# Optimization experiments

Hardware: AMD Instinct MI355X
Metric: run time of the kernel (lower is better)

## Reference

```python
import jax, jax.numpy as jnp
import numpy as np

P, N, C_IN, UNITS = 40000, 32, 4, 64
VX, VY = 0.2, 0.2
X_OFF = VX / 2 + 0.0      # pc_range x_min = 0
Y_OFF = VY / 2 + (-40.0)  # pc_range y_min = -40
BN_EPS = 1e-3


def setup_inputs() -> dict:
    key = jax.random.key(0)
    k1, k2, k3, k4, k5 = jax.random.split(key, 5)
    features = jax.random.normal(k1, (P, N, C_IN), dtype=jnp.float32)
    num_voxels = jax.random.randint(k2, (P,), 1, N + 1, dtype=jnp.int32)
    yx = jax.random.randint(k3, (P, 2), 0, 350, dtype=jnp.int32)
    coors = jnp.concatenate([jnp.zeros((P, 2), jnp.int32), yx], axis=1)  # (batch, z, y, x)
    W = jax.random.normal(k4, (C_IN + 5, UNITS), dtype=jnp.float32) * 0.1
    gamma = jnp.ones((UNITS,), jnp.float32)
    beta = jnp.zeros((UNITS,), jnp.float32)
    return {"features": features, "num_voxels": num_voxels, "coors": coors,
            "W": W, "gamma": gamma, "beta": beta}


def _pfn_forward(features, num_voxels, coors, W, gamma, beta):
    dtype = features.dtype
    nv = num_voxels.astype(dtype)[:, None, None]                      # [P,1,1]
    points_mean = jnp.sum(features[:, :, :3], axis=1, keepdims=True) / nv
    f_cluster = features[:, :, :3] - points_mean                      # [P,N,3]
    fx = features[:, :, 0] - (coors[:, 3].astype(dtype)[:, None] * VX + X_OFF)
    fy = features[:, :, 1] - (coors[:, 2].astype(dtype)[:, None] * VY + Y_OFF)
    f_center = jnp.stack([fx, fy], axis=-1)                           # [P,N,2]
    feats = jnp.concatenate([features, f_cluster, f_center], axis=-1) # [P,N,9]
    # mask out padded points (n >= num_voxels)
    mask = (jnp.arange(N)[None, :] < num_voxels[:, None]).astype(dtype)[..., None]
    feats = feats * mask
    # PFNLayer: linear (no bias) -> BN1d (training-mode batch stats) -> relu -> max over points
    x = jnp.einsum('pnc,cu->pnu', feats, W)                           # [P,N,U]
    mean = jnp.mean(x, axis=(0, 1))
    var = jnp.mean(jnp.square(x - mean), axis=(0, 1))                 # biased, as torch BN
    x = (x - mean) * jax.lax.rsqrt(var + BN_EPS) * gamma + beta
    x = jax.nn.relu(x)
    return jnp.max(x, axis=1)                                         # [P,U] (squeezed)


def reference(features, num_voxels, coors, W, gamma, beta):
    return _pfn_forward(features, num_voxels, coors, W, gamma, beta)
```

## Files before the change

kernel.cpp:

```cpp
#include <hip/hip_runtime.h>
#include <math.h>

#define NPTS   32
#define UNITS  64
#define PTOT   40000
#define NPAIRS (PTOT / 2)
#define SBLOCKS 2500
#define WPB     4
#define TOTW    (SBLOCKS * WPB)
#define PPW     (NPAIRS / TOTW)


__global__ __launch_bounds__(256)
void pfn_main(const float* __restrict__ feat,
              const int*   __restrict__ nvox,
              const int*   __restrict__ coors,
              const float* __restrict__ Wm,
              const float* __restrict__ gamma,
              float*       __restrict__ xext,
              float*       __restrict__ partials)
{
    __shared__ float ps[WPB][128];

    const int tid  = threadIdx.x;
    const int lane = tid & 63;
    const int wave = __builtin_amdgcn_readfirstlane(tid >> 6);
    const int gwave = blockIdx.x * WPB + wave;

    const float sg  = (gamma[lane] >= 0.f) ? 1.f : -1.f;
    const float w4 = sg * Wm[4 * UNITS + lane], w5 = sg * Wm[5 * UNITS + lane];
    const float w6 = sg * Wm[6 * UNITS + lane], w7 = sg * Wm[7 * UNITS + lane];
    const float w8 = sg * Wm[8 * UNITS + lane];
    const float wp0 = sg * Wm[0 * UNITS + lane] + w4 + w7;
    const float wp1 = sg * Wm[1 * UNITS + lane] + w5 + w8;
    const float wp2 = sg * Wm[2 * UNITS + lane] + w6;
    const float wp3 = sg * Wm[3 * UNITS + lane];

    float lsum = 0.f, lsq = 0.f;

    #pragma unroll
    for (int it = 0; it < PPW; ++it) {
        const int pair = it * TOTW + gwave;
        const int p0 = pair * 2;

        const float4 f4 = *reinterpret_cast<const float4*>(feat + (size_t)pair * 256 + lane * 4);
        float sx = f4.x, sy = f4.y, sz = f4.z;
        #pragma unroll
        for (int off = 1; off < 32; off <<= 1) {
            sx += __shfl_xor(sx, off);
            sy += __shfl_xor(sy, off);
            sz += __shfl_xor(sz, off);
        }

        int nvA = nvox[p0], nvB = nvox[p0 + 1];
        nvA = nvA < 1 ? 1 : (nvA > NPTS ? NPTS : nvA);
        nvB = nvB < 1 ? 1 : (nvB > NPTS ? NPTS : nvB);
        const float cxA = (float)coors[p0 * 4 + 3] * 0.2f + 0.1f;
        const float cyA = (float)coors[p0 * 4 + 2] * 0.2f + (-39.9f);
        const float cxB = (float)coors[p0 * 4 + 7] * 0.2f + 0.1f;
        const float cyB = (float)coors[p0 * 4 + 6] * 0.2f + (-39.9f);
        const float iA  = 1.f / (float)nvA,  iB  = 1.f / (float)nvB;
        const float mA0 = __shfl(sx, 0)  * iA, mA1 = __shfl(sy, 0)  * iA, mA2 = __shfl(sz, 0)  * iA;
        const float mB0 = __shfl(sx, 32) * iB, mB1 = __shfl(sy, 32) * iB, mB2 = __shfl(sz, 32) * iB;
        const float bA = -(mA0 * w4 + mA1 * w5 + mA2 * w6 + cxA * w7 + cyA * w8);
        const float bB = -(mB0 * w4 + mB1 * w5 + mB2 * w6 + cxB * w7 + cyB * w8);

        const float* fpA = feat + (size_t)p0 * 128;
        const float* fpB = fpA + 128;

        float mA = -3.4e38f, mB = -3.4e38f;
        const int nmin = nvA < nvB ? nvA : nvB;

        #pragma unroll 4
        for (int n = 0; n < nmin; ++n) {
            const float4 a  = *reinterpret_cast<const float4*>(fpA + n * 4);
            const float4 b4 = *reinterpret_cast<const float4*>(fpB + n * 4);
            const float xA = fmaf(a.x,  wp0, fmaf(a.y,  wp1, fmaf(a.z,  wp2, fmaf(a.w,  wp3, bA))));
            const float xB = fmaf(b4.x, wp0, fmaf(b4.y, wp1, fmaf(b4.z, wp2, fmaf(b4.w, wp3, bB))));
            lsum += xA; lsq = fmaf(xA, xA, lsq); mA = fmaxf(mA, xA);
            lsum += xB; lsq = fmaf(xB, xB, lsq); mB = fmaxf(mB, xB);
        }
        #pragma unroll 4
        for (int n = nmin; n < nvA; ++n) {
            const float4 a = *reinterpret_cast<const float4*>(fpA + n * 4);
            const float xA = fmaf(a.x, wp0, fmaf(a.y, wp1, fmaf(a.z, wp2, fmaf(a.w, wp3, bA))));
            lsum += xA; lsq = fmaf(xA, xA, lsq); mA = fmaxf(mA, xA);
        }
        #pragma unroll 4
        for (int n = nmin; n < nvB; ++n) {
            const float4 b4 = *reinterpret_cast<const float4*>(fpB + n * 4);
            const float xB = fmaf(b4.x, wp0, fmaf(b4.y, wp1, fmaf(b4.z, wp2, fmaf(b4.w, wp3, bB))));
            lsum += xB; lsq = fmaf(xB, xB, lsq); mB = fmaxf(mB, xB);
        }

        xext[(size_t)p0 * UNITS + lane]       = sg * mA;
        xext[(size_t)(p0 + 1) * UNITS + lane] = sg * mB;
    }

    ps[wave][lane]      = sg * lsum;
    ps[wave][64 + lane] = lsq;
    __syncthreads();
    if (tid < 128)
        partials[blockIdx.x * 128 + tid] = ps[0][tid] + ps[1][tid] + ps[2][tid] + ps[3][tid];
}

__global__ __launch_bounds__(256)
void pfn_finalize(const float* __restrict__ partials,
                  const float* __restrict__ gamma,
                  const float* __restrict__ beta,
                  float*       __restrict__ ss)
{
    const int u = blockIdx.x;
    const int t = threadIdx.x;
    double aS = 0.0, aQ = 0.0;
    for (int b = t; b < SBLOCKS; b += 256) {
        aS += (double)partials[b * 128 + u];
        aQ += (double)partials[b * 128 + 64 + u];
    }
    __shared__ double sS[256], sQ[256];
    sS[t] = aS; sQ[t] = aQ;
    __syncthreads();
    for (int s = 128; s > 0; s >>= 1) {
        if (t < s) { sS[t] += sS[t + s]; sQ[t] += sQ[t + s]; }
        __syncthreads();
    }
    if (t == 0) {
        const double inv_pn = 1.0 / ((double)PTOT * (double)NPTS);
        const double mean = sS[0] * inv_pn;
        const double var  = sQ[0] * inv_pn - mean * mean;
        const float scale = gamma[u] * (float)(1.0 / sqrt(var + 1e-3));
        const float shift = beta[u] - (float)mean * scale;
        ss[u]      = scale;
        ss[64 + u] = shift;
    }
}

#define CBLOCKS 2500

__global__ __launch_bounds__(256)
void pfn_apply(const float4* __restrict__ xext,
               const int*    __restrict__ nvox,
               const float*  __restrict__ ss,
               float4*       __restrict__ out)
{
    const int i  = blockIdx.x * 256 + threadIdx.x;
    const int u0 = (i & 15) * 4;
    const int p  = i >> 4;
    const float4 sc = *reinterpret_cast<const float4*>(ss + u0);
    const float4 sh = *reinterpret_cast<const float4*>(ss + 64 + u0);
    const float4 e  = xext[i];
    const bool pad  = nvox[p] < NPTS;
    float4 o;
    o.x = fmaxf(fmaf(e.x, sc.x, sh.x), pad ? fmaxf(sh.x, 0.f) : 0.f);
    o.y = fmaxf(fmaf(e.y, sc.y, sh.y), pad ? fmaxf(sh.y, 0.f) : 0.f);
    o.z = fmaxf(fmaf(e.z, sc.z, sh.z), pad ? fmaxf(sh.z, 0.f) : 0.f);
    o.w = fmaxf(fmaf(e.w, sc.w, sh.w), pad ? fmaxf(sh.w, 0.f) : 0.f);
    out[i] = o;
}

extern "C" void kernel_launch(void* const* d_in, const int* in_sizes, int n_in,
                              void* d_out, int out_size, void* d_ws, size_t ws_size,
                              hipStream_t stream)
{
    const float* feat  = (const float*)d_in[0];
    const int*   nvox  = (const int*)d_in[1];
    const int*   coors = (const int*)d_in[2];
    const float* Wm    = (const float*)d_in[3];
    const float* gamma = (const float*)d_in[4];
    const float* beta  = (const float*)d_in[5];
    float* out = (float*)d_out;

    float* xext     = (float*)d_ws;
    float* partials = xext + (size_t)PTOT * UNITS;
    float* ss       = partials + (size_t)SBLOCKS * 128;

    pfn_main<<<SBLOCKS, 256, 0, stream>>>(feat, nvox, coors, Wm, gamma, xext, partials);
    pfn_finalize<<<UNITS, 256, 0, stream>>>(partials, gamma, beta, ss);
    pfn_apply<<<CBLOCKS, 256, 0, stream>>>((const float4*)xext, nvox, ss, (float4*)out);
}
```

Baseline: 34.73 us.

## Use readlane from registers, atomic stat accumulation, fold finalize into apply

The per-point inner loops now pull each point's features out of the already-loaded float4 register with readlane, instead of reloading them from global memory. The separate finalize kernel is removed. Block partial sums go into a 128-float accumulator through float atomics, cleared by a memset before the main kernel, and each apply block computes scale and shift in shared memory. This drops a kernel launch and redundant loads, but adds a memset node and 2500×128 contended atomics. It also switches the statistics to float32 accumulation with E[x²]−mean², which loses precision compared with the earlier double reduction.

```diff
diff --git a/kernel.cpp b/kernel.cpp
--- a/kernel.cpp
+++ b/kernel.cpp
@@ -1,15 +1,19 @@
 #include <hip/hip_runtime.h>
 #include <math.h>
 
-#define NPTS   32
-#define UNITS  64
-#define PTOT   40000
-#define NPAIRS (PTOT / 2)
+#define NPTS    32
+#define UNITS   64
+#define PTOT    40000
+#define NPAIRS  (PTOT / 2)
 #define SBLOCKS 2500
 #define WPB     4
 #define TOTW    (SBLOCKS * WPB)
 #define PPW     (NPAIRS / TOTW)
 
+
+__device__ __forceinline__ float rl(float v, int srclane) {
+    return __int_as_float(__builtin_amdgcn_readlane(__float_as_int(v), srclane));
+}
 
 __global__ __launch_bounds__(256)
 void pfn_main(const float* __restrict__ feat,
@@ -18,7 +22,7 @@
               const float* __restrict__ Wm,
               const float* __restrict__ gamma,
               float*       __restrict__ xext,
-              float*       __restrict__ partials)
+              float*       __restrict__ accum)
 {
     __shared__ float ps[WPB][128];
 
@@ -44,6 +48,7 @@
         const int p0 = pair * 2;
 
         const float4 f4 = *reinterpret_cast<const float4*>(feat + (size_t)pair * 256 + lane * 4);
+
         float sx = f4.x, sy = f4.y, sz = f4.z;
         #pragma unroll
         for (int off = 1; off < 32; off <<= 1) {
@@ -60,36 +65,37 @@
         const float cxB = (float)coors[p0 * 4 + 7] * 0.2f + 0.1f;
         const float cyB = (float)coors[p0 * 4 + 6] * 0.2f + (-39.9f);
         const float iA  = 1.f / (float)nvA,  iB  = 1.f / (float)nvB;
-        const float mA0 = __shfl(sx, 0)  * iA, mA1 = __shfl(sy, 0)  * iA, mA2 = __shfl(sz, 0)  * iA;
-        const float mB0 = __shfl(sx, 32) * iB, mB1 = __shfl(sy, 32) * iB, mB2 = __shfl(sz, 32) * iB;
+        const float mA0 = rl(sx, 0)  * iA, mA1 = rl(sy, 0)  * iA, mA2 = rl(sz, 0)  * iA;
+        const float mB0 = rl(sx, 32) * iB, mB1 = rl(sy, 32) * iB, mB2 = rl(sz, 32) * iB;
         const float bA = -(mA0 * w4 + mA1 * w5 + mA2 * w6 + cxA * w7 + cyA * w8);
         const float bB = -(mB0 * w4 + mB1 * w5 + mB2 * w6 + cxB * w7 + cyB * w8);
-
-        const float* fpA = feat + (size_t)p0 * 128;
-        const float* fpB = fpA + 128;
 
         float mA = -3.4e38f, mB = -3.4e38f;
         const int nmin = nvA < nvB ? nvA : nvB;
 
         #pragma unroll 4
         for (int n = 0; n < nmin; ++n) {
-            const float4 a  = *reinterpret_cast<const float4*>(fpA + n * 4);
-            const float4 b4 = *reinterpret_cast<const float4*>(fpB + n * 4);
-            const float xA = fmaf(a.x,  wp0, fmaf(a.y,  wp1, fmaf(a.z,  wp2, fmaf(a.w,  wp3, bA))));
-            const float xB = fmaf(b4.x, wp0, fmaf(b4.y, wp1, fmaf(b4.z, wp2, fmaf(b4.w, wp3, bB))));
+            const float aX = rl(f4.x, n),      aY = rl(f4.y, n);
+            const float aZ = rl(f4.z, n),      aW = rl(f4.w, n);
+            const float bX = rl(f4.x, n + 32), bY = rl(f4.y, n + 32);
+            const float bZ = rl(f4.z, n + 32), bW = rl(f4.w, n + 32);
+            const float xA = fmaf(aX, wp0, fmaf(aY, wp1, fmaf(aZ, wp2, fmaf(aW, wp3, bA))));
+            const float xB = fmaf(bX, wp0, fmaf(bY, wp1, fmaf(bZ, wp2, fmaf(bW, wp3, bB))));
             lsum += xA; lsq = fmaf(xA, xA, lsq); mA = fmaxf(mA, xA);
             lsum += xB; lsq = fmaf(xB, xB, lsq); mB = fmaxf(mB, xB);
         }
         #pragma unroll 4
         for (int n = nmin; n < nvA; ++n) {
-            const float4 a = *reinterpret_cast<const float4*>(fpA + n * 4);
-            const float xA = fmaf(a.x, wp0, fmaf(a.y, wp1, fmaf(a.z, wp2, fmaf(a.w, wp3, bA))));
+            const float aX = rl(f4.x, n), aY = rl(f4.y, n);
+            const float aZ = rl(f4.z, n), aW = rl(f4.w, n);
+            const float xA = fmaf(aX, wp0, fmaf(aY, wp1, fmaf(aZ, wp2, fmaf(aW, wp3, bA))));
             lsum += xA; lsq = fmaf(xA, xA, lsq); mA = fmaxf(mA, xA);
         }
         #pragma unroll 4
         for (int n = nmin; n < nvB; ++n) {
-            const float4 b4 = *reinterpret_cast<const float4*>(fpB + n * 4);
-            const float xB = fmaf(b4.x, wp0, fmaf(b4.y, wp1, fmaf(b4.z, wp2, fmaf(b4.w, wp3, bB))));
+            const float bX = rl(f4.x, n + 32), bY = rl(f4.y, n + 32);
+            const float bZ = rl(f4.z, n + 32), bW = rl(f4.w, n + 32);
+            const float xB = fmaf(bX, wp0, fmaf(bY, wp1, fmaf(bZ, wp2, fmaf(bW, wp3, bB))));
             lsum += xB; lsq = fmaf(xB, xB, lsq); mB = fmaxf(mB, xB);
         }
 
@@ -100,54 +106,40 @@
     ps[wave][lane]      = sg * lsum;
     ps[wave][64 + lane] = lsq;
     __syncthreads();
-    if (tid < 128)
-        partials[blockIdx.x * 128 + tid] = ps[0][tid] + ps[1][tid] + ps[2][tid] + ps[3][tid];
-}
-
-__global__ __launch_bounds__(256)
-void pfn_finalize(const float* __restrict__ partials,
-                  const float* __restrict__ gamma,
-                  const float* __restrict__ beta,
-                  float*       __restrict__ ss)
-{
-    const int u = blockIdx.x;
-    const int t = threadIdx.x;
-    double aS = 0.0, aQ = 0.0;
-    for (int b = t; b < SBLOCKS; b += 256) {
-        aS += (double)partials[b * 128 + u];
-        aQ += (double)partials[b * 128 + 64 + u];
-    }
-    __shared__ double sS[256], sQ[256];
-    sS[t] = aS; sQ[t] = aQ;
-    __syncthreads();
-    for (int s = 128; s > 0; s >>= 1) {
-        if (t < s) { sS[t] += sS[t + s]; sQ[t] += sQ[t + s]; }
-        __syncthreads();
-    }
-    if (t == 0) {
-        const double inv_pn = 1.0 / ((double)PTOT * (double)NPTS);
-        const double mean = sS[0] * inv_pn;
-        const double var  = sQ[0] * inv_pn - mean * mean;
-        const float scale = gamma[u] * (float)(1.0 / sqrt(var + 1e-3));
-        const float shift = beta[u] - (float)mean * scale;
-        ss[u]      = scale;
-        ss[64 + u] = shift;
+    if (tid < 128) {
+        const float v = ps[0][tid] + ps[1][tid] + ps[2][tid] + ps[3][tid];
+        atomicAdd(&accum[tid], v);
     }
 }
 
 #define CBLOCKS 2500
 
 __global__ __launch_bounds__(256)
-void pfn_apply(const float4* __restrict__ xext,
+void pfn_apply(const float*  __restrict__ accum,
+               const float*  __restrict__ gamma,
+               const float*  __restrict__ beta,
+               const float4* __restrict__ xext,
                const int*    __restrict__ nvox,
-               const float*  __restrict__ ss,
                float4*       __restrict__ out)
 {
-    const int i  = blockIdx.x * 256 + threadIdx.x;
+    __shared__ __align__(16) float s_sc[64], s_sh[64];
+    const int t = threadIdx.x;
+    if (t < 64) {
+        const float INV_PN = 1.0f / (float)(PTOT * NPTS);
+        const float S = accum[t], Q = accum[64 + t];
+        const float mean  = S * INV_PN;
+        const float var   = Q * INV_PN - mean * mean;
+        const float scale = gamma[t] * rsqrtf(var + 1e-3f);
+        s_sc[t] = scale;
+        s_sh[t] = beta[t] - mean * scale;
+    }
+    __syncthreads();
+
+    const int i  = blockIdx.x * 256 + t;
     const int u0 = (i & 15) * 4;
     const int p  = i >> 4;
-    const float4 sc = *reinterpret_cast<const float4*>(ss + u0);
-    const float4 sh = *reinterpret_cast<const float4*>(ss + 64 + u0);
+    const float4 sc = *reinterpret_cast<const float4*>(&s_sc[u0]);
+    const float4 sh = *reinterpret_cast<const float4*>(&s_sh[u0]);
     const float4 e  = xext[i];
     const bool pad  = nvox[p] < NPTS;
     float4 o;
@@ -170,11 +162,11 @@
     const float* beta  = (const float*)d_in[5];
     float* out = (float*)d_out;
 
-    float* xext     = (float*)d_ws;
-    float* partials = xext + (size_t)PTOT * UNITS;
-    float* ss       = partials + (size_t)SBLOCKS * 128;
+    float* xext  = (float*)d_ws;
+    float* accum = xext + (size_t)PTOT * UNITS;
 
-    pfn_main<<<SBLOCKS, 256, 0, stream>>>(feat, nvox, coors, Wm, gamma, xext, partials);
-    pfn_finalize<<<UNITS, 256, 0, stream>>>(partials, gamma, beta, ss);
-    pfn_apply<<<CBLOCKS, 256, 0, stream>>>((const float4*)xext, nvox, ss, (float4*)out);
+    hipMemsetAsync(accum, 0, 128 * sizeof(float), stream);
+    pfn_main<<<SBLOCKS, 256, 0, stream>>>(feat, nvox, coors, Wm, gamma, xext, accum);
+    pfn_apply<<<CBLOCKS, 256, 0, stream>>>(accum, gamma, beta,
+                                           (const float4*)xext, nvox, (float4*)out);
 }
```

Result: slower. 83.56 us (+140.6%).

## Stage voxel points in LDS, prefetch metadata, and software-pipeline the point loop

Applied to the files above, without the earlier changes.

Each wave now writes the float4 feature block it already loaded into shared memory and reads the points back from LDS instead of re-reading them with broadcast global loads. All per-iteration loads (features, num_voxels, coors) are hoisted ahead of the compute loop. The point loop becomes a double-buffered four-point chunk loop that masks invalid points instead of running three separate min/tail loops. This costs extra LDS traffic, predicated work on padded points, and higher register pressure from the prefetch arrays.

```diff
diff --git a/kernel.cpp b/kernel.cpp
--- a/kernel.cpp
+++ b/kernel.cpp
@@ -1,10 +1,10 @@
 #include <hip/hip_runtime.h>
 #include <math.h>
 
-#define NPTS   32
-#define UNITS  64
-#define PTOT   40000
-#define NPAIRS (PTOT / 2)
+#define NPTS    32
+#define UNITS   64
+#define PTOT    40000
+#define NPAIRS  (PTOT / 2)
 #define SBLOCKS 2500
 #define WPB     4
 #define TOTW    (SBLOCKS * WPB)
@@ -20,12 +20,14 @@
               float*       __restrict__ xext,
               float*       __restrict__ partials)
 {
-    __shared__ float ps[WPB][128];
+    __shared__ float4 sf[WPB][2][NPTS];
+    __shared__ float  ps[WPB][128];
 
     const int tid  = threadIdx.x;
     const int lane = tid & 63;
     const int wave = __builtin_amdgcn_readfirstlane(tid >> 6);
     const int gwave = blockIdx.x * WPB + wave;
+    const int half = lane >> 5, pt = lane & 31;
 
     const float sg  = (gamma[lane] >= 0.f) ? 1.f : -1.f;
     const float w4 = sg * Wm[4 * UNITS + lane], w5 = sg * Wm[5 * UNITS + lane];
@@ -36,15 +38,33 @@
     const float wp2 = sg * Wm[2 * UNITS + lane] + w6;
     const float wp3 = sg * Wm[3 * UNITS + lane];
 
-    float lsum = 0.f, lsq = 0.f;
-
+    float4 fv[PPW];
+    int nvAv[PPW], nvBv[PPW];
+    float cxAv[PPW], cyAv[PPW], cxBv[PPW], cyBv[PPW];
     #pragma unroll
     for (int it = 0; it < PPW; ++it) {
         const int pair = it * TOTW + gwave;
         const int p0 = pair * 2;
-
-        const float4 f4 = *reinterpret_cast<const float4*>(feat + (size_t)pair * 256 + lane * 4);
-        float sx = f4.x, sy = f4.y, sz = f4.z;
+        fv[it] = *reinterpret_cast<const float4*>(feat + (size_t)pair * 256 + lane * 4);
+        int nvA = nvox[p0], nvB = nvox[p0 + 1];
+        nvAv[it] = nvA < 1 ? 1 : (nvA > NPTS ? NPTS : nvA);
+        nvBv[it] = nvB < 1 ? 1 : (nvB > NPTS ? NPTS : nvB);
+        cxAv[it] = (float)coors[p0 * 4 + 3] * 0.2f + 0.1f;
+        cyAv[it] = (float)coors[p0 * 4 + 2] * 0.2f + (-39.9f);
+        cxBv[it] = (float)coors[p0 * 4 + 7] * 0.2f + 0.1f;
+        cyBv[it] = (float)coors[p0 * 4 + 6] * 0.2f + (-39.9f);
+    }
+
+    float lsumA = 0.f, lsumB = 0.f, lsqA = 0.f, lsqB = 0.f;
+
+    #pragma unroll
+    for (int it = 0; it < PPW; ++it) {
+        const int pair = it * TOTW + gwave;
+        const int p0 = pair * 2;
+
+        sf[wave][half][pt] = fv[it];
+
+        float sx = fv[it].x, sy = fv[it].y, sz = fv[it].z;
         #pragma unroll
         for (int off = 1; off < 32; off <<= 1) {
             sx += __shfl_xor(sx, off);
@@ -52,53 +72,63 @@
             sz += __shfl_xor(sz, off);
         }
 
-        int nvA = nvox[p0], nvB = nvox[p0 + 1];
-        nvA = nvA < 1 ? 1 : (nvA > NPTS ? NPTS : nvA);
-        nvB = nvB < 1 ? 1 : (nvB > NPTS ? NPTS : nvB);
-        const float cxA = (float)coors[p0 * 4 + 3] * 0.2f + 0.1f;
-        const float cyA = (float)coors[p0 * 4 + 2] * 0.2f + (-39.9f);
-        const float cxB = (float)coors[p0 * 4 + 7] * 0.2f + 0.1f;
-        const float cyB = (float)coors[p0 * 4 + 6] * 0.2f + (-39.9f);
-        const float iA  = 1.f / (float)nvA,  iB  = 1.f / (float)nvB;
+        const int nvA = nvAv[it], nvB = nvBv[it];
+        const float iA = 1.f / (float)nvA, iB = 1.f / (float)nvB;
         const float mA0 = __shfl(sx, 0)  * iA, mA1 = __shfl(sy, 0)  * iA, mA2 = __shfl(sz, 0)  * iA;
         const float mB0 = __shfl(sx, 32) * iB, mB1 = __shfl(sy, 32) * iB, mB2 = __shfl(sz, 32) * iB;
-        const float bA = -(mA0 * w4 + mA1 * w5 + mA2 * w6 + cxA * w7 + cyA * w8);
-        const float bB = -(mB0 * w4 + mB1 * w5 + mB2 * w6 + cxB * w7 + cyB * w8);
-
-        const float* fpA = feat + (size_t)p0 * 128;
-        const float* fpB = fpA + 128;
+        const float bA = -(mA0 * w4 + mA1 * w5 + mA2 * w6 + cxAv[it] * w7 + cyAv[it] * w8);
+        const float bB = -(mB0 * w4 + mB1 * w5 + mB2 * w6 + cxBv[it] * w7 + cyBv[it] * w8);
 
         float mA = -3.4e38f, mB = -3.4e38f;
-        const int nmin = nvA < nvB ? nvA : nvB;
-
-        #pragma unroll 4
-        for (int n = 0; n < nmin; ++n) {
-            const float4 a  = *reinterpret_cast<const float4*>(fpA + n * 4);
-            const float4 b4 = *reinterpret_cast<const float4*>(fpB + n * 4);
-            const float xA = fmaf(a.x,  wp0, fmaf(a.y,  wp1, fmaf(a.z,  wp2, fmaf(a.w,  wp3, bA))));
-            const float xB = fmaf(b4.x, wp0, fmaf(b4.y, wp1, fmaf(b4.z, wp2, fmaf(b4.w, wp3, bB))));
-            lsum += xA; lsq = fmaf(xA, xA, lsq); mA = fmaxf(mA, xA);
-            lsum += xB; lsq = fmaf(xB, xB, lsq); mB = fmaxf(mB, xB);
-        }
-        #pragma unroll 4
-        for (int n = nmin; n < nvA; ++n) {
-            const float4 a = *reinterpret_cast<const float4*>(fpA + n * 4);
-            const float xA = fmaf(a.x, wp0, fmaf(a.y, wp1, fmaf(a.z, wp2, fmaf(a.w, wp3, bA))));
-            lsum += xA; lsq = fmaf(xA, xA, lsq); mA = fmaxf(mA, xA);
-        }
-        #pragma unroll 4
-        for (int n = nmin; n < nvB; ++n) {
-            const float4 b4 = *reinterpret_cast<const float4*>(fpB + n * 4);
-            const float xB = fmaf(b4.x, wp0, fmaf(b4.y, wp1, fmaf(b4.z, wp2, fmaf(b4.w, wp3, bB))));
-            lsum += xB; lsq = fmaf(xB, xB, lsq); mB = fmaxf(mB, xB);
+        const int nmax = nvA > nvB ? nvA : nvB;
+
+        float4 A0[4], B0[4], A1[4], B1[4];
+
+        auto compute = [&](int cbase, float4 (&A)[4], float4 (&B)[4]) {
+            #pragma unroll
+            for (int k = 0; k < 4; ++k) {
+                const int n = cbase + k;
+                const float4 a  = A[k];
+                const float4 b4 = B[k];
+                const float xA = fmaf(a.x,  wp0, fmaf(a.y,  wp1, fmaf(a.z,  wp2, fmaf(a.w,  wp3, bA))));
+                const float xB = fmaf(b4.x, wp0, fmaf(b4.y, wp1, fmaf(b4.z, wp2, fmaf(b4.w, wp3, bB))));
+                const float xAv = (n < nvA) ? xA : 0.f;
+                const float xBv = (n < nvB) ? xB : 0.f;
+                lsumA += xAv;  lsqA = fmaf(xAv, xA, lsqA);
+                lsumB += xBv;  lsqB = fmaf(xBv, xB, lsqB);
+                mA = fmaxf(mA, (n < nvA) ? xA : -3.4e38f);
+                mB = fmaxf(mB, (n < nvB) ? xB : -3.4e38f);
+            }
+        };
+
+        #pragma unroll
+        for (int k = 0; k < 4; ++k) { A0[k] = sf[wave][0][k]; B0[k] = sf[wave][1][k]; }
+        int c = 0;
+        while (true) {
+            const bool more = (c + 4 < nmax);
+            if (more) {
+                #pragma unroll
+                for (int k = 0; k < 4; ++k) { A1[k] = sf[wave][0][c + 4 + k]; B1[k] = sf[wave][1][c + 4 + k]; }
+            }
+            compute(c, A0, B0);
+            if (!more) break;
+            c += 4;
+            const bool more2 = (c + 4 < nmax);
+            if (more2) {
+                #pragma unroll
+                for (int k = 0; k < 4; ++k) { A0[k] = sf[wave][0][c + 4 + k]; B0[k] = sf[wave][1][c + 4 + k]; }
+            }
+            compute(c, A1, B1);
+            if (!more2) break;
+            c += 4;
         }
 
         xext[(size_t)p0 * UNITS + lane]       = sg * mA;
         xext[(size_t)(p0 + 1) * UNITS + lane] = sg * mB;
     }
 
-    ps[wave][lane]      = sg * lsum;
-    ps[wave][64 + lane] = lsq;
+    ps[wave][lane]      = sg * (lsumA + lsumB);
+    ps[wave][64 + lane] = lsqA + lsqB;
     __syncthreads();
     if (tid < 128)
         partials[blockIdx.x * 128 + tid] = ps[0][tid] + ps[1][tid] + ps[2][tid] + ps[3][tid];
@@ -138,9 +168,9 @@
 #define CBLOCKS 2500
 
 __global__ __launch_bounds__(256)
-void pfn_apply(const float4* __restrict__ xext,
+void pfn_apply(const float*  __restrict__ ss,
+               const float4* __restrict__ xext,
                const int*    __restrict__ nvox,
-               const float*  __restrict__ ss,
                float4*       __restrict__ out)
 {
     const int i  = blockIdx.x * 256 + threadIdx.x;
@@ -176,5 +206,5 @@
 
     pfn_main<<<SBLOCKS, 256, 0, stream>>>(feat, nvox, coors, Wm, gamma, xext, partials);
     pfn_finalize<<<UNITS, 256, 0, stream>>>(partials, gamma, beta, ss);
-    pfn_apply<<<CBLOCKS, 256, 0, stream>>>((const float4*)xext, nvox, ss, (float4*)out);
-}
+    pfn_apply<<<CBLOCKS, 256, 0, stream>>>(ss, (const float4*)xext, nvox, (float4*)out);
+}
```

Result: slower. 47.76 us (+37.5%).

## Compute per-voxel linear layer with bf16 MFMA including padded points

Applied to the files above, without the earlier changes.

Replaces the scalar per-lane FMA loop over valid points with bf16 32x32x16 MFMA instructions that compute all 32 points (padding zeroed) times 64 units per voxel. Padded rows now produce exact zeros, so the sum, sum-of-squares and max include them directly, and the apply kernel no longer reads num_voxels for the padding correction. This removes the data-dependent variable-length loops and the redundant per-lane feature loads. In exchange it rounds inputs and weights to bf16, which may exceed tolerance for the batch-norm statistics, and it adds shuffles and packing overhead per voxel.

```diff
diff --git a/kernel.cpp b/kernel.cpp
--- a/kernel.cpp
+++ b/kernel.cpp
@@ -1,15 +1,27 @@
 #include <hip/hip_runtime.h>
+#include <hip/hip_bf16.h>
 #include <math.h>
 
-#define NPTS   32
-#define UNITS  64
-#define PTOT   40000
-#define NPAIRS (PTOT / 2)
+#define NPTS    32
+#define UNITS   64
+#define PTOT    40000
+#define NPAIRS  (PTOT / 2)
 #define SBLOCKS 2500
 #define WPB     4
 #define TOTW    (SBLOCKS * WPB)
 #define PPW     (NPAIRS / TOTW)
 
+
+typedef __attribute__((ext_vector_type(8)))  short short8v;
+typedef __attribute__((ext_vector_type(16))) float f32x16;
+
+__device__ __forceinline__ unsigned short f2bf(float f) {
+    __hip_bfloat16 h = __float2bfloat16(f);
+    return *reinterpret_cast<unsigned short*>(&h);
+}
+__device__ __forceinline__ unsigned pk2(float lo, float hi) {
+    return ((unsigned)f2bf(hi) << 16) | (unsigned)f2bf(lo);
+}
 
 __global__ __launch_bounds__(256)
 void pfn_main(const float* __restrict__ feat,
@@ -26,15 +38,26 @@
     const int lane = tid & 63;
     const int wave = __builtin_amdgcn_readfirstlane(tid >> 6);
     const int gwave = blockIdx.x * WPB + wave;
-
-    const float sg  = (gamma[lane] >= 0.f) ? 1.f : -1.f;
-    const float w4 = sg * Wm[4 * UNITS + lane], w5 = sg * Wm[5 * UNITS + lane];
-    const float w6 = sg * Wm[6 * UNITS + lane], w7 = sg * Wm[7 * UNITS + lane];
-    const float w8 = sg * Wm[8 * UNITS + lane];
-    const float wp0 = sg * Wm[0 * UNITS + lane] + w4 + w7;
-    const float wp1 = sg * Wm[1 * UNITS + lane] + w5 + w8;
-    const float wp2 = sg * Wm[2 * UNITS + lane] + w6;
-    const float wp3 = sg * Wm[3 * UNITS + lane];
+    const int c31  = lane & 31;
+    const bool hiL = (lane >= 32);
+
+    short8v Bf[2];
+    #pragma unroll
+    for (int t = 0; t < 2; ++t) {
+        const int colg = 32 * t + c31;
+        const float sgc = (gamma[colg] >= 0.f) ? 1.f : -1.f;
+        const int k0 = hiL ? 8 : 0;
+        float bv[8];
+        #pragma unroll
+        for (int i = 0; i < 8; ++i) {
+            const int k = k0 + i;
+            bv[i] = (k < 9) ? sgc * Wm[k * UNITS + colg] : 0.f;
+        }
+        union { unsigned u[4]; short8v v; } B_;
+        B_.u[0] = pk2(bv[0], bv[1]); B_.u[1] = pk2(bv[2], bv[3]);
+        B_.u[2] = pk2(bv[4], bv[5]); B_.u[3] = pk2(bv[6], bv[7]);
+        Bf[t] = B_.v;
+    }
 
     float lsum = 0.f, lsq = 0.f;
 
@@ -44,6 +67,7 @@
         const int p0 = pair * 2;
 
         const float4 f4 = *reinterpret_cast<const float4*>(feat + (size_t)pair * 256 + lane * 4);
+
         float sx = f4.x, sy = f4.y, sz = f4.z;
         #pragma unroll
         for (int off = 1; off < 32; off <<= 1) {
@@ -52,52 +76,55 @@
             sz += __shfl_xor(sz, off);
         }
 
-        int nvA = nvox[p0], nvB = nvox[p0 + 1];
-        nvA = nvA < 1 ? 1 : (nvA > NPTS ? NPTS : nvA);
-        nvB = nvB < 1 ? 1 : (nvB > NPTS ? NPTS : nvB);
-        const float cxA = (float)coors[p0 * 4 + 3] * 0.2f + 0.1f;
-        const float cyA = (float)coors[p0 * 4 + 2] * 0.2f + (-39.9f);
-        const float cxB = (float)coors[p0 * 4 + 7] * 0.2f + 0.1f;
-        const float cyB = (float)coors[p0 * 4 + 6] * 0.2f + (-39.9f);
-        const float iA  = 1.f / (float)nvA,  iB  = 1.f / (float)nvB;
-        const float mA0 = __shfl(sx, 0)  * iA, mA1 = __shfl(sy, 0)  * iA, mA2 = __shfl(sz, 0)  * iA;
-        const float mB0 = __shfl(sx, 32) * iB, mB1 = __shfl(sy, 32) * iB, mB2 = __shfl(sz, 32) * iB;
-        const float bA = -(mA0 * w4 + mA1 * w5 + mA2 * w6 + cxA * w7 + cyA * w8);
-        const float bB = -(mB0 * w4 + mB1 * w5 + mB2 * w6 + cxB * w7 + cyB * w8);
-
-        const float* fpA = feat + (size_t)p0 * 128;
-        const float* fpB = fpA + 128;
-
-        float mA = -3.4e38f, mB = -3.4e38f;
-        const int nmin = nvA < nvB ? nvA : nvB;
-
-        #pragma unroll 4
-        for (int n = 0; n < nmin; ++n) {
-            const float4 a  = *reinterpret_cast<const float4*>(fpA + n * 4);
-            const float4 b4 = *reinterpret_cast<const float4*>(fpB + n * 4);
-            const float xA = fmaf(a.x,  wp0, fmaf(a.y,  wp1, fmaf(a.z,  wp2, fmaf(a.w,  wp3, bA))));
-            const float xB = fmaf(b4.x, wp0, fmaf(b4.y, wp1, fmaf(b4.z, wp2, fmaf(b4.w, wp3, bB))));
-            lsum += xA; lsq = fmaf(xA, xA, lsq); mA = fmaxf(mA, xA);
-            lsum += xB; lsq = fmaf(xB, xB, lsq); mB = fmaxf(mB, xB);
+        #pragma unroll
+        for (int h = 0; h < 2; ++h) {
+            const int p = p0 + h;
+            int nv = nvox[p]; nv = nv < 1 ? 1 : (nv > NPTS ? NPTS : nv);
+            const float cx = (float)coors[p * 4 + 3] * 0.2f + 0.1f;
+            const float cy = (float)coors[p * 4 + 2] * 0.2f + (-39.9f);
+            const float inv = 1.f / (float)nv;
+            const float m0 = __shfl(sx, 32 * h) * inv;
+            const float m1 = __shfl(sy, 32 * h) * inv;
+            const float m2 = __shfl(sz, 32 * h) * inv;
+
+            const int s = 32 * h + c31;
+            const float X = __shfl(f4.x, s), Y = __shfl(f4.y, s);
+            const float Z = __shfl(f4.z, s), I = __shfl(f4.w, s);
+
+            const unsigned lo0 = pk2(X, Y),        lo1 = pk2(Z, I);
+            const unsigned lo2 = pk2(X - m0, Y - m1), lo3 = pk2(Z - m2, X - cx);
+            const unsigned hi0 = pk2(Y - cy, 0.f);
+            const bool valid = (c31 < nv);
+            unsigned w0 = hiL ? hi0 : lo0;
+            unsigned w1 = hiL ? 0u : lo1;
+            unsigned w2 = hiL ? 0u : lo2;
+            unsigned w3 = hiL ? 0u : lo3;
+            union { unsigned u[4]; short8v v; } A_;
+            A_.u[0] = valid ? w0 : 0u; A_.u[1] = valid ? w1 : 0u;
+            A_.u[2] = valid ? w2 : 0u; A_.u[3] = valid ? w3 : 0u;
+
+            f32x16 c0 = {0,0,0,0,0,0,0,0,0,0,0,0,0,0,0,0};
+            f32x16 c1 = {0,0,0,0,0,0,0,0,0,0,0,0,0,0,0,0};
+            c0 = __builtin_amdgcn_mfma_f32_32x32x16_bf16(A_.v, Bf[0], c0, 0, 0, 0);
+            c1 = __builtin_amdgcn_mfma_f32_32x32x16_bf16(A_.v, Bf[1], c1, 0, 0, 0);
+
+            float s0 = 0.f, q0 = 0.f, x0m = -3.4e38f;
+            float s1 = 0.f, q1 = 0.f, x1m = -3.4e38f;
+            #pragma unroll
+            for (int r = 0; r < 16; ++r) {
+                const float x0 = c0[r], x1 = c1[r];
+                s0 += x0; q0 = fmaf(x0, x0, q0); x0m = fmaxf(x0m, x0);
+                s1 += x1; q1 = fmaf(x1, x1, q1); x1m = fmaxf(x1m, x1);
+            }
+            s0 += __shfl_xor(s0, 32); q0 += __shfl_xor(q0, 32); x0m = fmaxf(x0m, __shfl_xor(x0m, 32));
+            s1 += __shfl_xor(s1, 32); q1 += __shfl_xor(q1, 32); x1m = fmaxf(x1m, __shfl_xor(x1m, 32));
+            lsum += hiL ? s1 : s0;
+            lsq  += hiL ? q1 : q0;
+            xext[(size_t)p * UNITS + lane] = hiL ? x1m : x0m;
         }
-        #pragma unroll 4
-        for (int n = nmin; n < nvA; ++n) {
-            const float4 a = *reinterpret_cast<const float4*>(fpA + n * 4);
-            const float xA = fmaf(a.x, wp0, fmaf(a.y, wp1, fmaf(a.z, wp2, fmaf(a.w, wp3, bA))));
-            lsum += xA; lsq = fmaf(xA, xA, lsq); mA = fmaxf(mA, xA);
-        }
-        #pragma unroll 4
-        for (int n = nmin; n < nvB; ++n) {
-            const float4 b4 = *reinterpret_cast<const float4*>(fpB + n * 4);
-            const float xB = fmaf(b4.x, wp0, fmaf(b4.y, wp1, fmaf(b4.z, wp2, fmaf(b4.w, wp3, bB))));
-            lsum += xB; lsq = fmaf(xB, xB, lsq); mB = fmaxf(mB, xB);
-        }
-
-        xext[(size_t)p0 * UNITS + lane]       = sg * mA;
-        xext[(size_t)(p0 + 1) * UNITS + lane] = sg * mB;
-    }
-
-    ps[wave][lane]      = sg * lsum;
+    }
+
+    ps[wave][lane]      = lsum;
     ps[wave][64 + lane] = lsq;
     __syncthreads();
     if (tid < 128)
@@ -126,35 +153,31 @@
     }
     if (t == 0) {
         const double inv_pn = 1.0 / ((double)PTOT * (double)NPTS);
-        const double mean = sS[0] * inv_pn;
-        const double var  = sQ[0] * inv_pn - mean * mean;
-        const float scale = gamma[u] * (float)(1.0 / sqrt(var + 1e-3));
-        const float shift = beta[u] - (float)mean * scale;
-        ss[u]      = scale;
-        ss[64 + u] = shift;
+        const double meanp = sS[0] * inv_pn;
+        const double var   = sQ[0] * inv_pn - meanp * meanp;
+        const float  absc  = fabsf(gamma[u]) * (float)(1.0 / sqrt(var + 1e-3));
+        ss[u]      = absc;
+        ss[64 + u] = beta[u] - (float)meanp * absc;
     }
 }
 
 #define CBLOCKS 2500
 
 __global__ __launch_bounds__(256)
-void pfn_apply(const float4* __restrict__ xext,
-               const int*    __restrict__ nvox,
-               const float*  __restrict__ ss,
+void pfn_apply(const float*  __restrict__ ss,
+               const float4* __restrict__ xext,
                float4*       __restrict__ out)
 {
     const int i  = blockIdx.x * 256 + threadIdx.x;
     const int u0 = (i & 15) * 4;
-    const int p  = i >> 4;
     const float4 sc = *reinterpret_cast<const float4*>(ss + u0);
     const float4 sh = *reinterpret_cast<const float4*>(ss + 64 + u0);
     const float4 e  = xext[i];
-    const bool pad  = nvox[p] < NPTS;
     float4 o;
-    o.x = fmaxf(fmaf(e.x, sc.x, sh.x), pad ? fmaxf(sh.x, 0.f) : 0.f);
-    o.y = fmaxf(fmaf(e.y, sc.y, sh.y), pad ? fmaxf(sh.y, 0.f) : 0.f);
-    o.z = fmaxf(fmaf(e.z, sc.z, sh.z), pad ? fmaxf(sh.z, 0.f) : 0.f);
-    o.w = fmaxf(fmaf(e.w, sc.w, sh.w), pad ? fmaxf(sh.w, 0.f) : 0.f);
+    o.x = fmaxf(fmaf(e.x, sc.x, sh.x), 0.f);
+    o.y = fmaxf(fmaf(e.y, sc.y, sh.y), 0.f);
+    o.z = fmaxf(fmaf(e.z, sc.z, sh.z), 0.f);
+    o.w = fmaxf(fmaf(e.w, sc.w, sh.w), 0.f);
     out[i] = o;
 }
 
@@ -176,5 +199,5 @@
 
     pfn_main<<<SBLOCKS, 256, 0, stream>>>(feat, nvox, coors, Wm, gamma, xext, partials);
     pfn_finalize<<<UNITS, 256, 0, stream>>>(partials, gamma, beta, ss);
-    pfn_apply<<<CBLOCKS, 256, 0, stream>>>((const float4*)xext, nvox, ss, (float4*)out);
-}
+    pfn_apply<<<CBLOCKS, 256, 0, stream>>>(ss, (const float4*)xext, (float4*)out);
+}
```

New measurement: 39.72 us. 1.14x slower.
